# Kernel tuning notes

Hardware: AMD Instinct MI355X
Metric: run time of the kernel (lower is better)

The kernel has to match this reference:

```python
import jax, jax.numpy as jnp
import numpy as np

# Model dims (Llama-7B-like GQA)
S, B, D_MODEL = 2048, 2, 4096   # total seq, batch, hidden
NH, NKV, HD = 32, 8, 128        # q heads, kv heads, head dim
TP = 4                          # ring size -> number of KV blocks
SB = S // TP                    # KV block length per ring step


def setup_inputs() -> dict:
    key = jax.random.key(0)
    k1, k2, k3 = jax.random.split(key, 3)
    hidden_states = jax.random.normal(k1, (S, B, D_MODEL), jnp.float32)
    w_qkv = jax.random.normal(k2, (D_MODEL, (NH + 2 * NKV) * HD), jnp.float32) / np.sqrt(D_MODEL)
    w_o = jax.random.normal(k3, (NH * HD, D_MODEL), jnp.float32) / np.sqrt(NH * HD)
    return {"hidden_states": hidden_states, "w_qkv": w_qkv, "w_o": w_o}


def _ring_attention(hidden_states, w_qkv, w_o):
    # fused QKV projection: [S,B,D] @ [D,(NH+2*NKV)*HD]
    qkv = hidden_states @ w_qkv
    q, k, v = jnp.split(qkv, [NH * HD, (NH + NKV) * HD], axis=-1)
    q = q.reshape(S, B, NH, HD).transpose(1, 2, 0, 3)    # [B,NH,S,HD]
    k = k.reshape(S, B, NKV, HD).transpose(1, 2, 0, 3)   # [B,NKV,S,HD]
    v = v.reshape(S, B, NKV, HD).transpose(1, 2, 0, 3)

    groups = NH // NKV  # GQA: expand kv heads to match q heads
    k = jnp.repeat(k, groups, axis=1)  # [B,NH,S,HD]
    v = jnp.repeat(v, groups, axis=1)

    scale = 1.0 / np.sqrt(HD)

    # Split K/V along sequence into TP ring blocks: [TP,B,NH,SB,HD]
    k_blocks = k.reshape(B, NH, TP, SB, HD).transpose(2, 0, 1, 3, 4)
    v_blocks = v.reshape(B, NH, TP, SB, HD).transpose(2, 0, 1, 3, 4)

    # Online-softmax (flash-attention style) accumulation over ring steps.
    m0 = jnp.full((B, NH, S), -jnp.inf, q.dtype)   # running row max
    l0 = jnp.zeros((B, NH, S), q.dtype)            # running denom
    acc0 = jnp.zeros((B, NH, S, HD), q.dtype)      # running numerator

    def step(carry, kv):
        m, l, acc = carry
        kb, vb = kv  # [B,NH,SB,HD]
        s = jnp.einsum('bhqd,bhkd->bhqk', q, kb) * scale  # [B,NH,S,SB]
        m_new = jnp.maximum(m, s.max(-1))
        p = jnp.exp(s - m_new[..., None])
        alpha = jnp.exp(m - m_new)
        l = l * alpha + p.sum(-1)
        acc = acc * alpha[..., None] + jnp.einsum('bhqk,bhkd->bhqd', p, vb)
        return (m_new, l, acc), None

    (m, l, acc), _ = jax.lax.scan(step, (m0, l0, acc0), (k_blocks, v_blocks))
    attn = acc / l[..., None]  # [B,NH,S,HD]

    # [B,NH,S,HD] -> [S*B, NH*HD] -> o_proj -> [S,B,D]
    attn = attn.transpose(2, 0, 1, 3).reshape(S * B, NH * HD)
    return (attn @ w_o).reshape(S, B, D_MODEL)


def reference(hidden_states, w_qkv, w_o):
    return _ring_attention(hidden_states, w_qkv, w_o)
```

## Files before the change

### kernel.cpp

```cpp
#include <hip/hip_runtime.h>
#include <hip/hip_bf16.h>


typedef __bf16 bf16x8 __attribute__((ext_vector_type(8)));
typedef float f32x4 __attribute__((ext_vector_type(4)));
typedef unsigned short u16;
typedef u16 u16x4 __attribute__((ext_vector_type(4)));
typedef u16 u16x8 __attribute__((ext_vector_type(8)));
typedef unsigned int u32;

#define SEQ    2048
#define BATCH  2
#define NROWS  4096
#define DM     4096
#define QKVC   6144
#define QSCALE (0.08838834764831845f * 1.4426950408889634f)

__device__ __forceinline__ u16 f2bf(float f) {
  union { float f; u32 u; } v; v.f = f;
  u32 r = v.u + 0x7fffu + ((v.u >> 16) & 1u);
  return (u16)(r >> 16);
}

__device__ __forceinline__ void gload16(const void* g, void* l) {
  __builtin_amdgcn_global_load_lds(
      (const __attribute__((address_space(1))) unsigned int*)g,
      (__attribute__((address_space(3))) unsigned int*)l, 16, 0, 0);
}

__device__ __forceinline__ void wg_barrier() {
  __builtin_amdgcn_sched_barrier(0);
  __builtin_amdgcn_s_barrier();
  __builtin_amdgcn_sched_barrier(0);
}

__global__ __launch_bounds__(256) void conv_f32_bf16(
    const float* __restrict__ in, u16* __restrict__ out) {
  size_t i = ((size_t)blockIdx.x * 256 + threadIdx.x) * 8;
  float4 a = *(const float4*)(in + i);
  float4 b = *(const float4*)(in + i + 4);
  u16x8 o;
  o[0] = f2bf(a.x); o[1] = f2bf(a.y); o[2] = f2bf(a.z); o[3] = f2bf(a.w);
  o[4] = f2bf(b.x); o[5] = f2bf(b.y); o[6] = f2bf(b.z); o[7] = f2bf(b.w);
  *(u16x8*)(out + i) = o;
}

__global__ __launch_bounds__(256) void transpose_f32_bf16(
    const float* __restrict__ in, u16* __restrict__ out, int K, int N) {
  __shared__ u16 tile[64][65];
  const int k0 = blockIdx.y * 64, n0 = blockIdx.x * 64;
  const int t = threadIdx.x;
#pragma unroll
  for (int i = 0; i < 4; ++i) {
    int slot = i * 256 + t;
    int r = slot >> 4, cq = slot & 15;
    float4 v = *(const float4*)(in + (size_t)(k0 + r) * N + n0 + cq * 4);
    tile[cq * 4 + 0][r] = f2bf(v.x);
    tile[cq * 4 + 1][r] = f2bf(v.y);
    tile[cq * 4 + 2][r] = f2bf(v.z);
    tile[cq * 4 + 3][r] = f2bf(v.w);
  }
  __syncthreads();
#pragma unroll
  for (int i = 0; i < 2; ++i) {
    int slot = i * 256 + t;
    int n = slot >> 3, q = slot & 7;
    u16x8 o;
#pragma unroll
    for (int e = 0; e < 8; ++e) o[e] = tile[n][q * 8 + e];
    *(u16x8*)(out + (size_t)(n0 + n) * K + k0 + q * 8) = o;
  }
}

__global__ __launch_bounds__(256) void vtrans(
    const u16* __restrict__ qkv, u16* __restrict__ vt) {
  __shared__ u16 tile[64][66];
  const int s0 = blockIdx.x * 64, d0 = blockIdx.y * 64;
  const int z = blockIdx.z;
  const int b = z >> 3, kvh = z & 7;
  const int t = threadIdx.x;
#pragma unroll
  for (int i = 0; i < 2; ++i) {
    int chunk = i * 256 + t;
    int r = chunk >> 3, q = chunk & 7;
    u16x8 v = *(const u16x8*)&qkv[(size_t)((s0 + r) * 2 + b) * QKVC + 5120 + kvh * 128 + d0 + q * 8];
#pragma unroll
    for (int e = 0; e < 8; ++e) tile[r][q * 8 + e] = v[e];
  }
  __syncthreads();
#pragma unroll
  for (int i = 0; i < 2; ++i) {
    int chunk = i * 256 + t;
    int d = chunk >> 3, q = chunk & 7;
    u16x8 o;
#pragma unroll
    for (int e = 0; e < 8; ++e) o[e] = tile[q * 8 + e][d];
    *(u16x8*)&vt[(size_t)(z * 128 + d0 + d) * SEQ + s0 + q * 8] = o;
  }
}

template <int CBF16, int SCALEQ>
__global__ __launch_bounds__(512, 2) void gemm192(
    const u16* __restrict__ A, const u16* __restrict__ B,
    void* __restrict__ C, int M, int N, int K, int nby) {
  __shared__ u16 As[2 * 16384];
  __shared__ u16 Bs[2 * 12288];
  const int t = threadIdx.x;
  const int w = t >> 6, l = t & 63;
  const int g = l >> 4, c = l & 15;
  const int wm = w >> 2, wn = w & 3;

  const int nwg = gridDim.x;
  const int sid = (blockIdx.x & 7) * (nwg >> 3) + (blockIdx.x >> 3);
  const int by = sid % nby, bx = sid / nby;
  const int m0 = by * 256, n0 = bx * 192;

  const int gsrc = (l & 7) ^ (l >> 3);
  const u16* pA = A + (size_t)(m0 + w * 8 + (l >> 3)) * K + gsrc * 8;
  const u16* pB = B + (size_t)(n0 + w * 8 + (l >> 3)) * K + gsrc * 8;

#define STG_A192(tt) do { int d_ = (tt) & 1;                                \
    _Pragma("unroll")                                                       \
    for (int u = 0; u < 4; ++u)                                             \
      gload16(pA + (size_t)(u * 64) * K + (size_t)(tt) * 64,                \
              &As[d_ * 16384 + u * 4096 + w * 512]); } while (0)
#define STG_B192(tt) do { int d_ = (tt) & 1;                                \
    _Pragma("unroll")                                                       \
    for (int u = 0; u < 3; ++u)                                             \
      gload16(pB + (size_t)(u * 64) * K + (size_t)(tt) * 64,                \
              &Bs[d_ * 12288 + u * 4096 + w * 512]); } while (0)

  const int xr0 = ((0 + g) ^ (c & 7)) << 3;
  const int xr1 = ((4 + g) ^ (c & 7)) << 3;

  const f32x4 fz = {0.f, 0.f, 0.f, 0.f};
  f32x4 acc[8][3];
#pragma unroll
  for (int m = 0; m < 8; ++m)
#pragma unroll
    for (int n = 0; n < 3; ++n) acc[m][n] = fz;

  const int nkt = K >> 6;
  STG_A192(0); STG_B192(0); STG_B192(1);
  asm volatile("s_waitcnt vmcnt(3)" ::: "memory");
  __builtin_amdgcn_sched_barrier(0);
  __builtin_amdgcn_s_barrier();

  for (int tt = 0; tt < nkt; ++tt) {
    const int d = tt & 1;
    const u16* aT = &As[d * 16384 + (wm * 128 + c) * 64];
    const u16* bT = &Bs[d * 12288 + (wn * 48 + c) * 64];
    bf16x8 av[4][2], bv[3][2];

#pragma unroll
    for (int m = 0; m < 4; ++m) {
      av[m][0] = *(const bf16x8*)(aT + m * 1024 + xr0);
      av[m][1] = *(const bf16x8*)(aT + m * 1024 + xr1);
    }
#pragma unroll
    for (int n = 0; n < 3; ++n) {
      bv[n][0] = *(const bf16x8*)(bT + n * 1024 + xr0);
      bv[n][1] = *(const bf16x8*)(bT + n * 1024 + xr1);
    }
    if (tt + 1 < nkt) STG_A192(tt + 1);
    __builtin_amdgcn_s_barrier();
    __builtin_amdgcn_s_setprio(1);
#pragma unroll
    for (int kk = 0; kk < 2; ++kk)
#pragma unroll
      for (int m = 0; m < 4; ++m)
#pragma unroll
        for (int n = 0; n < 3; ++n)
          acc[m][n] = __builtin_amdgcn_mfma_f32_16x16x32_bf16(
              av[m][kk], bv[n][kk], acc[m][n], 0, 0, 0);
    __builtin_amdgcn_s_setprio(0);
    __builtin_amdgcn_s_barrier();

#pragma unroll
    for (int m = 0; m < 4; ++m) {
      av[m][0] = *(const bf16x8*)(aT + (4 + m) * 1024 + xr0);
      av[m][1] = *(const bf16x8*)(aT + (4 + m) * 1024 + xr1);
    }
    if (tt + 2 < nkt) {
      STG_B192(tt + 2);
      asm volatile("s_waitcnt vmcnt(3)" ::: "memory");
    } else {
      asm volatile("s_waitcnt vmcnt(0)" ::: "memory");
    }
    __builtin_amdgcn_sched_barrier(0);
    __builtin_amdgcn_s_barrier();
    __builtin_amdgcn_s_setprio(1);
#pragma unroll
    for (int kk = 0; kk < 2; ++kk)
#pragma unroll
      for (int m = 0; m < 4; ++m)
#pragma unroll
        for (int n = 0; n < 3; ++n)
          acc[4 + m][n] = __builtin_amdgcn_mfma_f32_16x16x32_bf16(
              av[m][kk], bv[n][kk], acc[4 + m][n], 0, 0, 0);
    __builtin_amdgcn_s_setprio(0);
    __builtin_amdgcn_s_barrier();
  }
#undef STG_A192
#undef STG_B192

#pragma unroll
  for (int m = 0; m < 8; ++m)
#pragma unroll
    for (int n = 0; n < 3; ++n) {
      int row = m0 + wm * 128 + m * 16 + g * 4;
      int col = n0 + wn * 48 + n * 16 + c;
      float sc = (SCALEQ && col < 4096) ? QSCALE : 1.0f;
#pragma unroll
      for (int r = 0; r < 4; ++r) {
        float x = acc[m][n][r] * sc;
        if (CBF16) ((u16*)C)[(size_t)(row + r) * N + col] = f2bf(x);
        else       ((float*)C)[(size_t)(row + r) * N + col] = x;
      }
    }
}

template <int CBF16, int SCALEQ>
__global__ __launch_bounds__(512, 2) void gemm256(
    const u16* __restrict__ A, const u16* __restrict__ B,
    void* __restrict__ C, int M, int N, int K, int nby) {
  __shared__ u16 As[2 * 2 * 8192];
  __shared__ u16 Bs[2 * 2 * 8192];
  const int t = threadIdx.x;
  const int w = t >> 6, l = t & 63;
  const int g = l >> 4, c = l & 15;
  const int wm = w >> 2, wn = w & 3;

  const int nwg = gridDim.x;
  const int sid = (blockIdx.x & 7) * (nwg >> 3) + (blockIdx.x >> 3);
  const int by = sid % nby, bx = sid / nby;
  const int m0 = by * 256, n0 = bx * 256;

  const int gsrc = (l & 7) ^ (l >> 3);
  const u16* pA = A + (size_t)(m0 + w * 8 + (l >> 3)) * K + gsrc * 8;
  const u16* pB = B + (size_t)(n0 + w * 8 + (l >> 3)) * K + gsrc * 8;

#define STG_A(h, tt) do { int d_ = (tt) & 1;                                    \
    gload16(pA + (size_t)((h) * 128) * K + (tt) * 64,                           \
            &As[(d_ * 2 + (h)) * 8192 + w * 512]);                              \
    gload16(pA + (size_t)((h) * 128 + 64) * K + (tt) * 64,                      \
            &As[(d_ * 2 + (h)) * 8192 + 4096 + w * 512]); } while (0)
#define STG_B(h, tt) do { int d_ = (tt) & 1;                                    \
    gload16(pB + (size_t)((h) * 128) * K + (tt) * 64,                           \
            &Bs[(d_ * 2 + (h)) * 8192 + w * 512]);                              \
    gload16(pB + (size_t)((h) * 128 + 64) * K + (tt) * 64,                      \
            &Bs[(d_ * 2 + (h)) * 8192 + 4096 + w * 512]); } while (0)

  const u16* aRd = &As[wm * 8192 + c * 64];
  const u16* bRd = &Bs[(wn >> 1) * 8192 + ((wn & 1) * 64 + c) * 64];
  const int xr0 = ((0 + g) ^ (c & 7)) << 3;
  const int xr1 = ((4 + g) ^ (c & 7)) << 3;

  const f32x4 fz = {0.f, 0.f, 0.f, 0.f};
  f32x4 acc[8][4];
#pragma unroll
  for (int mi = 0; mi < 8; ++mi)
#pragma unroll
    for (int nj = 0; nj < 4; ++nj) acc[mi][nj] = fz;

  const int nkt = K >> 6;
  STG_A(0, 0); STG_A(1, 0); STG_B(0, 0); STG_B(1, 0);
  STG_B(0, 1); STG_B(1, 1);
  asm volatile("s_waitcnt vmcnt(4)" ::: "memory");
  __builtin_amdgcn_sched_barrier(0);
  wg_barrier();

  for (int tt = 0; tt < nkt; ++tt) {
    const int d = tt & 1;
    const u16* aT = aRd + d * 16384;
    const u16* bT = bRd + d * 16384;
    bf16x8 av[4][2], b01[2][2], b23[2][2];

#pragma unroll
    for (int m = 0; m < 4; ++m) {
      av[m][0] = *(const bf16x8*)(aT + m * 1024 + xr0);
      av[m][1] = *(const bf16x8*)(aT + m * 1024 + xr1);
    }
#pragma unroll
    for (int n = 0; n < 2; ++n) {
      b01[n][0] = *(const bf16x8*)(bT + n * 1024 + xr0);
      b01[n][1] = *(const bf16x8*)(bT + n * 1024 + xr1);
    }
    if (tt + 1 < nkt) STG_A(0, tt + 1);
    wg_barrier();
    __builtin_amdgcn_s_setprio(1);
#pragma unroll
    for (int kk = 0; kk < 2; ++kk)
#pragma unroll
      for (int m = 0; m < 4; ++m)
#pragma unroll
        for (int n = 0; n < 2; ++n)
          acc[m][n] = __builtin_amdgcn_mfma_f32_16x16x32_bf16(
              av[m][kk], b01[n][kk], acc[m][n], 0, 0, 0);
    __builtin_amdgcn_s_setprio(0);
    wg_barrier();

#pragma unroll
    for (int n = 0; n < 2; ++n) {
      b23[n][0] = *(const bf16x8*)(bT + (2 + n) * 1024 + xr0);
      b23[n][1] = *(const bf16x8*)(bT + (2 + n) * 1024 + xr1);
    }
    if (tt + 1 < nkt) STG_A(1, tt + 1);
    wg_barrier();
    __builtin_amdgcn_s_setprio(1);
#pragma unroll
    for (int kk = 0; kk < 2; ++kk)
#pragma unroll
      for (int m = 0; m < 4; ++m)
#pragma unroll
        for (int n = 0; n < 2; ++n)
          acc[m][2 + n] = __builtin_amdgcn_mfma_f32_16x16x32_bf16(
              av[m][kk], b23[n][kk], acc[m][2 + n], 0, 0, 0);
    __builtin_amdgcn_s_setprio(0);
    wg_barrier();

#pragma unroll
    for (int m = 0; m < 4; ++m) {
      av[m][0] = *(const bf16x8*)(aT + (4 + m) * 1024 + xr0);
      av[m][1] = *(const bf16x8*)(aT + (4 + m) * 1024 + xr1);
    }
    if (tt + 2 < nkt) STG_B(0, tt + 2);
    wg_barrier();
    __builtin_amdgcn_s_setprio(1);
#pragma unroll
    for (int kk = 0; kk < 2; ++kk)
#pragma unroll
      for (int m = 0; m < 4; ++m)
#pragma unroll
        for (int n = 0; n < 2; ++n)
          acc[4 + m][2 + n] = __builtin_amdgcn_mfma_f32_16x16x32_bf16(
              av[m][kk], b23[n][kk], acc[4 + m][2 + n], 0, 0, 0);
    __builtin_amdgcn_s_setprio(0);
    wg_barrier();

    if (tt + 2 < nkt) STG_B(1, tt + 2);
    if (tt < nkt - 2) asm volatile("s_waitcnt vmcnt(4)" ::: "memory");
    else              asm volatile("s_waitcnt vmcnt(0)" ::: "memory");
    __builtin_amdgcn_sched_barrier(0);
    wg_barrier();
    __builtin_amdgcn_s_setprio(1);
#pragma unroll
    for (int kk = 0; kk < 2; ++kk)
#pragma unroll
      for (int m = 0; m < 4; ++m)
#pragma unroll
        for (int n = 0; n < 2; ++n)
          acc[4 + m][n] = __builtin_amdgcn_mfma_f32_16x16x32_bf16(
              av[m][kk], b01[n][kk], acc[4 + m][n], 0, 0, 0);
    __builtin_amdgcn_s_setprio(0);
    wg_barrier();
  }
#undef STG_A
#undef STG_B

#pragma unroll
  for (int mi = 0; mi < 8; ++mi)
#pragma unroll
    for (int nj = 0; nj < 4; ++nj) {
      int row = m0 + wm * 128 + mi * 16 + g * 4;
      int col = n0 + wn * 64 + nj * 16 + c;
      float sc = (SCALEQ && col < 4096) ? QSCALE : 1.0f;
#pragma unroll
      for (int r = 0; r < 4; ++r) {
        float x = acc[mi][nj][r] * sc;
        if (CBF16) ((u16*)C)[(size_t)(row + r) * N + col] = f2bf(x);
        else       ((float*)C)[(size_t)(row + r) * N + col] = x;
      }
    }
}

__global__ __launch_bounds__(512, 4) void attn_fwd2(
    const u16* __restrict__ qkv, const u16* __restrict__ vtg,
    u16* __restrict__ out) {
  __shared__ u16 Ks[2][64 * 128];
  __shared__ u16 Vs[2][128 * 64];
  __shared__ u16 Ps[8][16 * 64];
  const int t = threadIdx.x;
  const int w = t >> 6, lane = t & 63;
  const int g = lane >> 4, c = lane & 15;
  const int bh = blockIdx.y;
  const int b = bh >> 5, h = bh & 31, kvh = h >> 2;
  const int q0 = blockIdx.x * 128 + w * 16;

  bf16x8 qf[4];
#pragma unroll
  for (int kk = 0; kk < 4; ++kk)
    qf[kk] = *(const bf16x8*)&qkv[(size_t)((q0 + c) * 2 + b) * QKVC + h * 128 + kk * 32 + g * 8];

  const f32x4 fz = {0.f, 0.f, 0.f, 0.f};
  f32x4 acc[8];
#pragma unroll
  for (int db = 0; db < 8; ++db) acc[db] = fz;
  float m_ = -__builtin_inff(), l_ = 0.f;

  const int w4g = w * 4 + g;
  const u16* pK = qkv + (size_t)b * QKVC + 4096 + kvh * 128 + (size_t)((c ^ w4g) & 15) * 8;
  const int vrow = w * 8 + (lane >> 3);
  const u16* pV = vtg + (size_t)(b * 8 + kvh) * 128 * SEQ + (size_t)((lane & 7) ^ (lane >> 3)) * 8;

  auto stage = [&](int bufi, int kv0) {
#pragma unroll
    for (int j = 0; j < 2; ++j)
      gload16(pK + (size_t)(kv0 + j * 32 + w4g) * (2 * QKVC), &Ks[bufi][(j * 8 + w) * 512]);
#pragma unroll
    for (int j = 0; j < 2; ++j)
      gload16(pV + (size_t)(j * 64 + vrow) * SEQ + kv0, &Vs[bufi][(j * 8 + w) * 512]);
  };

  stage(0, 0);
  int buf = 0;
  for (int kv0 = 0; kv0 < SEQ; kv0 += 64) {
    __syncthreads();
    if (kv0 + 64 < SEQ) stage(buf ^ 1, kv0 + 64);

    f32x4 st[4];
    __builtin_amdgcn_s_setprio(1);
#pragma unroll
    for (int kf = 0; kf < 4; ++kf) {
      const u16* kr = &Ks[buf][(kf * 16 + c) * 128];
      bf16x8 kfr[4];
#pragma unroll
      for (int kk = 0; kk < 4; ++kk)
        kfr[kk] = *(const bf16x8*)&kr[(((kk * 4 + g) ^ c) & 15) * 8];
      f32x4 s = fz;
#pragma unroll
      for (int kk = 0; kk < 4; ++kk)
        s = __builtin_amdgcn_mfma_f32_16x16x32_bf16(kfr[kk], qf[kk], s, 0, 0, 0);
      st[kf] = s;
    }
    __builtin_amdgcn_s_setprio(0);

    float mloc = st[0][0];
#pragma unroll
    for (int kf = 0; kf < 4; ++kf)
#pragma unroll
      for (int r = 0; r < 4; ++r) mloc = fmaxf(mloc, st[kf][r]);
    mloc = fmaxf(mloc, __shfl_xor(mloc, 16));
    mloc = fmaxf(mloc, __shfl_xor(mloc, 32));
    if (!__all(mloc - m_ <= 8.0f)) {
      float mnew = fmaxf(m_, mloc);
      float alpha = __builtin_amdgcn_exp2f(m_ - mnew);
      l_ *= alpha;
      f32x4 av;
#pragma unroll
      for (int r = 0; r < 4; ++r) av[r] = __shfl(alpha, g * 4 + r);
#pragma unroll
      for (int db = 0; db < 8; ++db) acc[db] *= av;
      m_ = mnew;
    }
    float ps = 0.f;
#pragma unroll
    for (int kf = 0; kf < 4; ++kf) {
      u16x4 pk;
#pragma unroll
      for (int r = 0; r < 4; ++r) {
        float p = __builtin_amdgcn_exp2f(st[kf][r] - m_);
        ps += p;
        pk[r] = f2bf(p);
      }
      *(u16x4*)&Ps[w][c * 64 + ((((kf * 2 + (g >> 1)) ^ (c & 7)) << 3) | ((g & 1) << 2))] = pk;
    }
    ps += __shfl_xor(ps, 16);
    ps += __shfl_xor(ps, 32);
    l_ += ps;

    bf16x8 pa0 = *(const bf16x8*)&Ps[w][c * 64 + (((0 + g) ^ (c & 7)) << 3)];
    bf16x8 pa1 = *(const bf16x8*)&Ps[w][c * 64 + (((4 + g) ^ (c & 7)) << 3)];
    __builtin_amdgcn_s_setprio(1);
#pragma unroll
    for (int db = 0; db < 8; ++db) {
      const u16* vr = &Vs[buf][(db * 16 + c) * 64];
      bf16x8 v0 = *(const bf16x8*)&vr[(((0 + g) ^ (c & 7)) << 3)];
      bf16x8 v1 = *(const bf16x8*)&vr[(((4 + g) ^ (c & 7)) << 3)];
      acc[db] = __builtin_amdgcn_mfma_f32_16x16x32_bf16(pa0, v0, acc[db], 0, 0, 0);
      acc[db] = __builtin_amdgcn_mfma_f32_16x16x32_bf16(pa1, v1, acc[db], 0, 0, 0);
    }
    __builtin_amdgcn_s_setprio(0);
    buf ^= 1;
  }

  float linv = __builtin_amdgcn_rcpf(l_);
  f32x4 il;
#pragma unroll
  for (int r = 0; r < 4; ++r) il[r] = __shfl(linv, g * 4 + r);
#pragma unroll
  for (int db = 0; db < 8; ++db) {
#pragma unroll
    for (int r = 0; r < 4; ++r) {
      int s = q0 + g * 4 + r;
      out[(size_t)(s * 2 + b) * DM + h * 128 + db * 16 + c] = f2bf(acc[db][r] * il[r]);
    }
  }
}

extern "C" void kernel_launch(void* const* d_in, const int* in_sizes, int n_in,
                              void* d_out, int out_size, void* d_ws, size_t ws_size,
                              hipStream_t stream) {
  const float* hidden = (const float*)d_in[0];
  const float* w_qkv  = (const float*)d_in[1];
  const float* w_o    = (const float*)d_in[2];
  float* outp = (float*)d_out;

  const size_t SZ_X  = (size_t)NROWS * DM * 2;
  const size_t SZ_WQ = (size_t)QKVC * DM * 2;
  const size_t SZ_WO = (size_t)DM * DM * 2;
  const size_t SZ_QKV = (size_t)NROWS * QKVC * 2;
  if (ws_size < SZ_X + SZ_WQ + SZ_WO + SZ_QKV) return;

  char* ws = (char*)d_ws;
  u16* Xb    = (u16*)ws;
  u16* WqkvT = (u16*)(ws + SZ_X);
  u16* WoT   = (u16*)(ws + SZ_X + SZ_WQ);
  u16* QKVb  = (u16*)(ws + SZ_X + SZ_WQ + SZ_WO);
  u16* VtG   = WqkvT;
  u16* Attn  = Xb;

  conv_f32_bf16<<<(NROWS * (size_t)DM) / 2048, 256, 0, stream>>>(hidden, Xb);
  transpose_f32_bf16<<<dim3(QKVC / 64, DM / 64), 256, 0, stream>>>(w_qkv, WqkvT, DM, QKVC);
  transpose_f32_bf16<<<dim3(DM / 64, DM / 64), 256, 0, stream>>>(w_o, WoT, DM, DM);
  gemm192<1, 1><<<512, 512, 0, stream>>>(Xb, WqkvT, QKVb, NROWS, QKVC, DM, 16);
  vtrans<<<dim3(SEQ / 64, 2, 16), 256, 0, stream>>>(QKVb, VtG);
  attn_fwd2<<<dim3(SEQ / 128, BATCH * 32), 512, 0, stream>>>(QKVb, VtG, Attn);
  gemm256<0, 0><<<256, 512, 0, stream>>>(Attn, WoT, outp, NROWS, DM, DM, 16);
}
```

Before: 533.8 us.

## Triple-buffer A tiles in gemm192 and drop sched barriers around s_barrier

The gemm192 kernel now keeps three LDS buffers for the A operand and prefetches A two k-tiles ahead instead of one, with wait counts adjusted to match. This aims to hide more global-load latency behind the MFMA work. The MFMA loops are reordered so all first-half-k products issue before second-half-k products. In the other GEMM, the wg_barrier helper (s_barrier wrapped by sched_barrier fences) is replaced with a bare s_barrier, giving the compiler more scheduling freedom. The extra A buffer raises LDS use per block, which may reduce occupancy under launch_bounds(512,2).

```diff
diff --git a/kernel.cpp b/kernel.cpp
--- a/kernel.cpp
+++ b/kernel.cpp
@@ -26,12 +26,6 @@
   __builtin_amdgcn_global_load_lds(
       (const __attribute__((address_space(1))) unsigned int*)g,
       (__attribute__((address_space(3))) unsigned int*)l, 16, 0, 0);
-}
-
-__device__ __forceinline__ void wg_barrier() {
-  __builtin_amdgcn_sched_barrier(0);
-  __builtin_amdgcn_s_barrier();
-  __builtin_amdgcn_sched_barrier(0);
 }
 
 __global__ __launch_bounds__(256) void conv_f32_bf16(
@@ -103,7 +97,7 @@
 __global__ __launch_bounds__(512, 2) void gemm192(
     const u16* __restrict__ A, const u16* __restrict__ B,
     void* __restrict__ C, int M, int N, int K, int nby) {
-  __shared__ u16 As[2 * 16384];
+  __shared__ u16 As[3 * 16384];
   __shared__ u16 Bs[2 * 12288];
   const int t = threadIdx.x;
   const int w = t >> 6, l = t & 63;
@@ -119,11 +113,11 @@
   const u16* pA = A + (size_t)(m0 + w * 8 + (l >> 3)) * K + gsrc * 8;
   const u16* pB = B + (size_t)(n0 + w * 8 + (l >> 3)) * K + gsrc * 8;
 
-#define STG_A192(tt) do { int d_ = (tt) & 1;                                \
+#define STG_A192(tt, bb) do {                                               \
     _Pragma("unroll")                                                       \
     for (int u = 0; u < 4; ++u)                                             \
       gload16(pA + (size_t)(u * 64) * K + (size_t)(tt) * 64,                \
-              &As[d_ * 16384 + u * 4096 + w * 512]); } while (0)
+              &As[(bb) * 16384 + u * 4096 + w * 512]); } while (0)
 #define STG_B192(tt) do { int d_ = (tt) & 1;                                \
     _Pragma("unroll")                                                       \
     for (int u = 0; u < 3; ++u)                                             \
@@ -141,49 +135,57 @@
     for (int n = 0; n < 3; ++n) acc[m][n] = fz;
 
   const int nkt = K >> 6;
-  STG_A192(0); STG_B192(0); STG_B192(1);
-  asm volatile("s_waitcnt vmcnt(3)" ::: "memory");
+  STG_A192(0, 0); STG_B192(0);
+  STG_A192(1, 1); STG_B192(1);
+  asm volatile("s_waitcnt vmcnt(7)" ::: "memory");
   __builtin_amdgcn_sched_barrier(0);
   __builtin_amdgcn_s_barrier();
 
+  int ab = 0;
   for (int tt = 0; tt < nkt; ++tt) {
-    const int d = tt & 1;
-    const u16* aT = &As[d * 16384 + (wm * 128 + c) * 64];
-    const u16* bT = &Bs[d * 12288 + (wn * 48 + c) * 64];
-    bf16x8 av[4][2], bv[3][2];
+    const u16* aT = &As[ab * 16384 + (wm * 128 + c) * 64];
+    const u16* bT = &Bs[(tt & 1) * 12288 + (wn * 48 + c) * 64];
+    bf16x8 a0[4], a1[4], bv[3][2];
 
 #pragma unroll
     for (int m = 0; m < 4; ++m) {
-      av[m][0] = *(const bf16x8*)(aT + m * 1024 + xr0);
-      av[m][1] = *(const bf16x8*)(aT + m * 1024 + xr1);
+      a0[m] = *(const bf16x8*)(aT + m * 1024 + xr0);
+      a1[m] = *(const bf16x8*)(aT + m * 1024 + xr1);
     }
 #pragma unroll
     for (int n = 0; n < 3; ++n) {
       bv[n][0] = *(const bf16x8*)(bT + n * 1024 + xr0);
       bv[n][1] = *(const bf16x8*)(bT + n * 1024 + xr1);
     }
-    if (tt + 1 < nkt) STG_A192(tt + 1);
-    __builtin_amdgcn_s_barrier();
-    __builtin_amdgcn_s_setprio(1);
-#pragma unroll
-    for (int kk = 0; kk < 2; ++kk)
-#pragma unroll
-      for (int m = 0; m < 4; ++m)
-#pragma unroll
-        for (int n = 0; n < 3; ++n)
-          acc[m][n] = __builtin_amdgcn_mfma_f32_16x16x32_bf16(
-              av[m][kk], bv[n][kk], acc[m][n], 0, 0, 0);
+    {
+      int ab2 = ab + 2; if (ab2 >= 3) ab2 -= 3;
+      if (tt + 2 < nkt) STG_A192(tt + 2, ab2);
+    }
+    __builtin_amdgcn_s_barrier();
+    __builtin_amdgcn_s_setprio(1);
+#pragma unroll
+    for (int m = 0; m < 4; ++m)
+#pragma unroll
+      for (int n = 0; n < 3; ++n)
+        acc[m][n] = __builtin_amdgcn_mfma_f32_16x16x32_bf16(
+            a0[m], bv[n][0], acc[m][n], 0, 0, 0);
+#pragma unroll
+    for (int m = 0; m < 4; ++m)
+#pragma unroll
+      for (int n = 0; n < 3; ++n)
+        acc[m][n] = __builtin_amdgcn_mfma_f32_16x16x32_bf16(
+            a1[m], bv[n][1], acc[m][n], 0, 0, 0);
     __builtin_amdgcn_s_setprio(0);
     __builtin_amdgcn_s_barrier();
 
 #pragma unroll
     for (int m = 0; m < 4; ++m) {
-      av[m][0] = *(const bf16x8*)(aT + (4 + m) * 1024 + xr0);
-      av[m][1] = *(const bf16x8*)(aT + (4 + m) * 1024 + xr1);
+      a0[m] = *(const bf16x8*)(aT + (4 + m) * 1024 + xr0);
+      a1[m] = *(const bf16x8*)(aT + (4 + m) * 1024 + xr1);
     }
     if (tt + 2 < nkt) {
       STG_B192(tt + 2);
-      asm volatile("s_waitcnt vmcnt(3)" ::: "memory");
+      asm volatile("s_waitcnt vmcnt(7)" ::: "memory");
     } else {
       asm volatile("s_waitcnt vmcnt(0)" ::: "memory");
     }
@@ -191,15 +193,20 @@
     __builtin_amdgcn_s_barrier();
     __builtin_amdgcn_s_setprio(1);
 #pragma unroll
-    for (int kk = 0; kk < 2; ++kk)
-#pragma unroll
-      for (int m = 0; m < 4; ++m)
-#pragma unroll
-        for (int n = 0; n < 3; ++n)
-          acc[4 + m][n] = __builtin_amdgcn_mfma_f32_16x16x32_bf16(
-              av[m][kk], bv[n][kk], acc[4 + m][n], 0, 0, 0);
-    __builtin_amdgcn_s_setprio(0);
-    __builtin_amdgcn_s_barrier();
+    for (int m = 0; m < 4; ++m)
+#pragma unroll
+      for (int n = 0; n < 3; ++n)
+        acc[4 + m][n] = __builtin_amdgcn_mfma_f32_16x16x32_bf16(
+            a0[m], bv[n][0], acc[4 + m][n], 0, 0, 0);
+#pragma unroll
+    for (int m = 0; m < 4; ++m)
+#pragma unroll
+      for (int n = 0; n < 3; ++n)
+        acc[4 + m][n] = __builtin_amdgcn_mfma_f32_16x16x32_bf16(
+            a1[m], bv[n][1], acc[4 + m][n], 0, 0, 0);
+    __builtin_amdgcn_s_setprio(0);
+    __builtin_amdgcn_s_barrier();
+    ab = (ab == 2) ? 0 : ab + 1;
   }
 #undef STG_A192
 #undef STG_B192
@@ -268,7 +275,7 @@
   STG_B(0, 1); STG_B(1, 1);
   asm volatile("s_waitcnt vmcnt(4)" ::: "memory");
   __builtin_amdgcn_sched_barrier(0);
-  wg_barrier();
+  __builtin_amdgcn_s_barrier();
 
   for (int tt = 0; tt < nkt; ++tt) {
     const int d = tt & 1;
@@ -287,7 +294,7 @@
       b01[n][1] = *(const bf16x8*)(bT + n * 1024 + xr1);
     }
     if (tt + 1 < nkt) STG_A(0, tt + 1);
-    wg_barrier();
+    __builtin_amdgcn_s_barrier();
     __builtin_amdgcn_s_setprio(1);
 #pragma unroll
     for (int kk = 0; kk < 2; ++kk)
@@ -298,7 +305,7 @@
           acc[m][n] = __builtin_amdgcn_mfma_f32_16x16x32_bf16(
               av[m][kk], b01[n][kk], acc[m][n], 0, 0, 0);
     __builtin_amdgcn_s_setprio(0);
-    wg_barrier();
+    __builtin_amdgcn_s_barrier();
 
 #pragma unroll
     for (int n = 0; n < 2; ++n) {
@@ -306,7 +313,7 @@
       b23[n][1] = *(const bf16x8*)(bT + (2 + n) * 1024 + xr1);
     }
     if (tt + 1 < nkt) STG_A(1, tt + 1);
-    wg_barrier();
+    __builtin_amdgcn_s_barrier();
     __builtin_amdgcn_s_setprio(1);
 #pragma unroll
     for (int kk = 0; kk < 2; ++kk)
@@ -317,7 +324,7 @@
           acc[m][2 + n] = __builtin_amdgcn_mfma_f32_16x16x32_bf16(
               av[m][kk], b23[n][kk], acc[m][2 + n], 0, 0, 0);
     __builtin_amdgcn_s_setprio(0);
-    wg_barrier();
+    __builtin_amdgcn_s_barrier();
 
 #pragma unroll
     for (int m = 0; m < 4; ++m) {
@@ -325,7 +332,7 @@
       av[m][1] = *(const bf16x8*)(aT + (4 + m) * 1024 + xr1);
     }
     if (tt + 2 < nkt) STG_B(0, tt + 2);
-    wg_barrier();
+    __builtin_amdgcn_s_barrier();
     __builtin_amdgcn_s_setprio(1);
 #pragma unroll
     for (int kk = 0; kk < 2; ++kk)
@@ -336,13 +343,13 @@
           acc[4 + m][2 + n] = __builtin_amdgcn_mfma_f32_16x16x32_bf16(
               av[m][kk], b23[n][kk], acc[4 + m][2 + n], 0, 0, 0);
     __builtin_amdgcn_s_setprio(0);
-    wg_barrier();
+    __builtin_amdgcn_s_barrier();
 
     if (tt + 2 < nkt) STG_B(1, tt + 2);
     if (tt < nkt - 2) asm volatile("s_waitcnt vmcnt(4)" ::: "memory");
     else              asm volatile("s_waitcnt vmcnt(0)" ::: "memory");
     __builtin_amdgcn_sched_barrier(0);
-    wg_barrier();
+    __builtin_amdgcn_s_barrier();
     __builtin_amdgcn_s_setprio(1);
 #pragma unroll
     for (int kk = 0; kk < 2; ++kk)
@@ -353,7 +360,7 @@
           acc[4 + m][n] = __builtin_amdgcn_mfma_f32_16x16x32_bf16(
               av[m][kk], b01[n][kk], acc[4 + m][n], 0, 0, 0);
     __builtin_amdgcn_s_setprio(0);
-    wg_barrier();
+    __builtin_amdgcn_s_barrier();
   }
 #undef STG_A
 #undef STG_B
```

Result: no change. 534.8 us (+0.2%).

## Shrink QKV GEMM tile to 128x192 with simpler double-buffered pipeline

Applied to the files above, without the earlier changes.

The QKV projection GEMM switches from a 256x192 tile to a 128x192 tile. The grid doubles to 1024 workgroups and the occupancy hint rises to 4. The K loop is rebuilt as a single-phase double buffer: it prefetches the next A and B tiles together, waits, then runs one MFMA block per iteration, replacing the split A/B staging schedule. The aim is more parallelism and occupancy, at the cost of lower operand reuse and more global traffic per FLOP. Separately, the gemm256 wg_barrier wrappers are replaced by plain s_barrier, dropping the sched_barrier fences around them, which changes how the compiler may schedule instructions.

```diff
diff --git a/kernel.cpp b/kernel.cpp
--- a/kernel.cpp
+++ b/kernel.cpp
@@ -26,12 +26,6 @@
   __builtin_amdgcn_global_load_lds(
       (const __attribute__((address_space(1))) unsigned int*)g,
       (__attribute__((address_space(3))) unsigned int*)l, 16, 0, 0);
-}
-
-__device__ __forceinline__ void wg_barrier() {
-  __builtin_amdgcn_sched_barrier(0);
-  __builtin_amdgcn_s_barrier();
-  __builtin_amdgcn_sched_barrier(0);
 }
 
 __global__ __launch_bounds__(256) void conv_f32_bf16(
@@ -100,10 +94,10 @@
 }
 
 template <int CBF16, int SCALEQ>
-__global__ __launch_bounds__(512, 2) void gemm192(
+__global__ __launch_bounds__(512, 4) void gemm128(
     const u16* __restrict__ A, const u16* __restrict__ B,
     void* __restrict__ C, int M, int N, int K, int nby) {
-  __shared__ u16 As[2 * 16384];
+  __shared__ u16 As[2 * 8192];
   __shared__ u16 Bs[2 * 12288];
   const int t = threadIdx.x;
   const int w = t >> 6, l = t & 63;
@@ -113,18 +107,17 @@
   const int nwg = gridDim.x;
   const int sid = (blockIdx.x & 7) * (nwg >> 3) + (blockIdx.x >> 3);
   const int by = sid % nby, bx = sid / nby;
-  const int m0 = by * 256, n0 = bx * 192;
+  const int m0 = by * 128, n0 = bx * 192;
 
   const int gsrc = (l & 7) ^ (l >> 3);
   const u16* pA = A + (size_t)(m0 + w * 8 + (l >> 3)) * K + gsrc * 8;
   const u16* pB = B + (size_t)(n0 + w * 8 + (l >> 3)) * K + gsrc * 8;
 
-#define STG_A192(tt) do { int d_ = (tt) & 1;                                \
+#define STG128(tt) do { int d_ = (tt) & 1;                                  \
     _Pragma("unroll")                                                       \
-    for (int u = 0; u < 4; ++u)                                             \
+    for (int u = 0; u < 2; ++u)                                             \
       gload16(pA + (size_t)(u * 64) * K + (size_t)(tt) * 64,                \
-              &As[d_ * 16384 + u * 4096 + w * 512]); } while (0)
-#define STG_B192(tt) do { int d_ = (tt) & 1;                                \
+              &As[d_ * 8192 + u * 4096 + w * 512]);                         \
     _Pragma("unroll")                                                       \
     for (int u = 0; u < 3; ++u)                                             \
       gload16(pB + (size_t)(u * 64) * K + (size_t)(tt) * 64,                \
@@ -134,24 +127,28 @@
   const int xr1 = ((4 + g) ^ (c & 7)) << 3;
 
   const f32x4 fz = {0.f, 0.f, 0.f, 0.f};
-  f32x4 acc[8][3];
-#pragma unroll
-  for (int m = 0; m < 8; ++m)
+  f32x4 acc[4][3];
+#pragma unroll
+  for (int m = 0; m < 4; ++m)
 #pragma unroll
     for (int n = 0; n < 3; ++n) acc[m][n] = fz;
 
   const int nkt = K >> 6;
-  STG_A192(0); STG_B192(0); STG_B192(1);
-  asm volatile("s_waitcnt vmcnt(3)" ::: "memory");
-  __builtin_amdgcn_sched_barrier(0);
-  __builtin_amdgcn_s_barrier();
-
+  STG128(0);
   for (int tt = 0; tt < nkt; ++tt) {
     const int d = tt & 1;
-    const u16* aT = &As[d * 16384 + (wm * 128 + c) * 64];
+    if (tt + 1 < nkt) {
+      STG128(tt + 1);
+      asm volatile("s_waitcnt vmcnt(5)" ::: "memory");
+    } else {
+      asm volatile("s_waitcnt vmcnt(0)" ::: "memory");
+    }
+    __builtin_amdgcn_sched_barrier(0);
+    __builtin_amdgcn_s_barrier();
+
+    const u16* aT = &As[d * 8192 + (wm * 64 + c) * 64];
     const u16* bT = &Bs[d * 12288 + (wn * 48 + c) * 64];
     bf16x8 av[4][2], bv[3][2];
-
 #pragma unroll
     for (int m = 0; m < 4; ++m) {
       av[m][0] = *(const bf16x8*)(aT + m * 1024 + xr0);
@@ -162,8 +159,6 @@
       bv[n][0] = *(const bf16x8*)(bT + n * 1024 + xr0);
       bv[n][1] = *(const bf16x8*)(bT + n * 1024 + xr1);
     }
-    if (tt + 1 < nkt) STG_A192(tt + 1);
-    __builtin_amdgcn_s_barrier();
     __builtin_amdgcn_s_setprio(1);
 #pragma unroll
     for (int kk = 0; kk < 2; ++kk)
@@ -175,40 +170,14 @@
               av[m][kk], bv[n][kk], acc[m][n], 0, 0, 0);
     __builtin_amdgcn_s_setprio(0);
     __builtin_amdgcn_s_barrier();
-
-#pragma unroll
-    for (int m = 0; m < 4; ++m) {
-      av[m][0] = *(const bf16x8*)(aT + (4 + m) * 1024 + xr0);
-      av[m][1] = *(const bf16x8*)(aT + (4 + m) * 1024 + xr1);
-    }
-    if (tt + 2 < nkt) {
-      STG_B192(tt + 2);
-      asm volatile("s_waitcnt vmcnt(3)" ::: "memory");
-    } else {
-      asm volatile("s_waitcnt vmcnt(0)" ::: "memory");
-    }
-    __builtin_amdgcn_sched_barrier(0);
-    __builtin_amdgcn_s_barrier();
-    __builtin_amdgcn_s_setprio(1);
-#pragma unroll
-    for (int kk = 0; kk < 2; ++kk)
-#pragma unroll
-      for (int m = 0; m < 4; ++m)
-#pragma unroll
-        for (int n = 0; n < 3; ++n)
-          acc[4 + m][n] = __builtin_amdgcn_mfma_f32_16x16x32_bf16(
-              av[m][kk], bv[n][kk], acc[4 + m][n], 0, 0, 0);
-    __builtin_amdgcn_s_setprio(0);
-    __builtin_amdgcn_s_barrier();
-  }
-#undef STG_A192
-#undef STG_B192
-
-#pragma unroll
-  for (int m = 0; m < 8; ++m)
+  }
+#undef STG128
+
+#pragma unroll
+  for (int m = 0; m < 4; ++m)
 #pragma unroll
     for (int n = 0; n < 3; ++n) {
-      int row = m0 + wm * 128 + m * 16 + g * 4;
+      int row = m0 + wm * 64 + m * 16 + g * 4;
       int col = n0 + wn * 48 + n * 16 + c;
       float sc = (SCALEQ && col < 4096) ? QSCALE : 1.0f;
 #pragma unroll
@@ -268,7 +237,7 @@
   STG_B(0, 1); STG_B(1, 1);
   asm volatile("s_waitcnt vmcnt(4)" ::: "memory");
   __builtin_amdgcn_sched_barrier(0);
-  wg_barrier();
+  __builtin_amdgcn_s_barrier();
 
   for (int tt = 0; tt < nkt; ++tt) {
     const int d = tt & 1;
@@ -287,7 +256,7 @@
       b01[n][1] = *(const bf16x8*)(bT + n * 1024 + xr1);
     }
     if (tt + 1 < nkt) STG_A(0, tt + 1);
-    wg_barrier();
+    __builtin_amdgcn_s_barrier();
     __builtin_amdgcn_s_setprio(1);
 #pragma unroll
     for (int kk = 0; kk < 2; ++kk)
@@ -298,7 +267,7 @@
           acc[m][n] = __builtin_amdgcn_mfma_f32_16x16x32_bf16(
               av[m][kk], b01[n][kk], acc[m][n], 0, 0, 0);
     __builtin_amdgcn_s_setprio(0);
-    wg_barrier();
+    __builtin_amdgcn_s_barrier();
 
 #pragma unroll
     for (int n = 0; n < 2; ++n) {
@@ -306,7 +275,7 @@
       b23[n][1] = *(const bf16x8*)(bT + (2 + n) * 1024 + xr1);
     }
     if (tt + 1 < nkt) STG_A(1, tt + 1);
-    wg_barrier();
+    __builtin_amdgcn_s_barrier();
     __builtin_amdgcn_s_setprio(1);
 #pragma unroll
     for (int kk = 0; kk < 2; ++kk)
@@ -317,7 +286,7 @@
           acc[m][2 + n] = __builtin_amdgcn_mfma_f32_16x16x32_bf16(
               av[m][kk], b23[n][kk], acc[m][2 + n], 0, 0, 0);
     __builtin_amdgcn_s_setprio(0);
-    wg_barrier();
+    __builtin_amdgcn_s_barrier();
 
 #pragma unroll
     for (int m = 0; m < 4; ++m) {
@@ -325,7 +294,7 @@
       av[m][1] = *(const bf16x8*)(aT + (4 + m) * 1024 + xr1);
     }
     if (tt + 2 < nkt) STG_B(0, tt + 2);
-    wg_barrier();
+    __builtin_amdgcn_s_barrier();
     __builtin_amdgcn_s_setprio(1);
 #pragma unroll
     for (int kk = 0; kk < 2; ++kk)
@@ -336,13 +305,13 @@
           acc[4 + m][2 + n] = __builtin_amdgcn_mfma_f32_16x16x32_bf16(
               av[m][kk], b23[n][kk], acc[4 + m][2 + n], 0, 0, 0);
     __builtin_amdgcn_s_setprio(0);
-    wg_barrier();
+    __builtin_amdgcn_s_barrier();
 
     if (tt + 2 < nkt) STG_B(1, tt + 2);
     if (tt < nkt - 2) asm volatile("s_waitcnt vmcnt(4)" ::: "memory");
     else              asm volatile("s_waitcnt vmcnt(0)" ::: "memory");
     __builtin_amdgcn_sched_barrier(0);
-    wg_barrier();
+    __builtin_amdgcn_s_barrier();
     __builtin_amdgcn_s_setprio(1);
 #pragma unroll
     for (int kk = 0; kk < 2; ++kk)
@@ -353,7 +322,7 @@
           acc[4 + m][n] = __builtin_amdgcn_mfma_f32_16x16x32_bf16(
               av[m][kk], b01[n][kk], acc[4 + m][n], 0, 0, 0);
     __builtin_amdgcn_s_setprio(0);
-    wg_barrier();
+    __builtin_amdgcn_s_barrier();
   }
 #undef STG_A
 #undef STG_B
@@ -523,7 +492,7 @@
   conv_f32_bf16<<<(NROWS * (size_t)DM) / 2048, 256, 0, stream>>>(hidden, Xb);
   transpose_f32_bf16<<<dim3(QKVC / 64, DM / 64), 256, 0, stream>>>(w_qkv, WqkvT, DM, QKVC);
   transpose_f32_bf16<<<dim3(DM / 64, DM / 64), 256, 0, stream>>>(w_o, WoT, DM, DM);
-  gemm192<1, 1><<<512, 512, 0, stream>>>(Xb, WqkvT, QKVb, NROWS, QKVC, DM, 16);
+  gemm128<1, 1><<<1024, 512, 0, stream>>>(Xb, WqkvT, QKVb, NROWS, QKVC, DM, 32);
   vtrans<<<dim3(SEQ / 64, 2, 16), 256, 0, stream>>>(QKVb, VtG);
   attn_fwd2<<<dim3(SEQ / 128, BATCH * 32), 512, 0, stream>>>(QKVb, VtG, Attn);
   gemm256<0, 0><<<256, 512, 0, stream>>>(Attn, WoT, outp, NROWS, DM, DM, 16);
```

New measurement: 532.7 us, median of 3. Within noise of the previous version (-0.2%).
